# Performance work log

Hardware: AMD Instinct MI355X
Metric: run time of the kernel (lower is better)

The kernel has to match this reference:

```python
import jax, jax.numpy as jnp
import numpy as np

B, NB, NA, F = 4, 262144, 8192, 32

def _mk_mlp(key, d_in):
    ks = jax.random.split(key, 3)
    def lin(k, i, o):
        bound = 1.0 / np.sqrt(i)
        kw, kb = jax.random.split(k)
        w = jax.random.uniform(kw, (i, o), jnp.float32, -bound, bound)
        b = jax.random.uniform(kb, (o,), jnp.float32, -bound, bound)
        return w, b
    w1, b1 = lin(ks[0], d_in, 64)
    w2, b2 = lin(ks[1], 64, 64)
    w3, b3 = lin(ks[2], 64, 32)
    return w1, b1, w2, b2, w3, b3

def setup_inputs() -> dict:
    key = jax.random.key(0)
    ks = jax.random.split(key, 8)
    inp = {
        "bonds": jax.random.normal(ks[0], (B, NB, F), jnp.float32),
        "bond_atom_1": jax.random.randint(ks[1], (B, NB), 0, NA, jnp.int32),
        "bond_atom_2": jax.random.randint(ks[2], (B, NB), 0, NA, jnp.int32),
        "atoms": jax.random.normal(ks[3], (B, NA, F), jnp.float32),
        "state": jax.random.normal(ks[4], (B, 1, F), jnp.float32),
    }
    for name, d_in, k in (("e", 128, ks[5]), ("v", 96, ks[6]), ("u", 96, ks[7])):
        w1, b1, w2, b2, w3, b3 = _mk_mlp(k, d_in)
        inp[f"{name}_w1"], inp[f"{name}_b1"] = w1, b1
        inp[f"{name}_w2"], inp[f"{name}_b2"] = w2, b2
        inp[f"{name}_w3"], inp[f"{name}_b3"] = w3, b3
    return inp

def _mlp(x, w1, b1, w2, b2, w3, b3):
    sp = jax.nn.softplus
    h = sp(x @ w1 + b1)
    h = sp(h @ w2 + b2)
    return sp(h @ w3 + b3)

def reference(bonds, bond_atom_1, bond_atom_2, atoms, state,
              e_w1, e_b1, e_w2, e_b2, e_w3, e_b3,
              v_w1, v_b1, v_w2, v_b2, v_w3, v_b3,
              u_w1, u_b1, u_w2, u_b2, u_w3, u_b3):
    num_atoms = atoms.shape[1]
    num_bonds = bonds.shape[1]
    # gather atom features to bonds: [B, NB, F]
    a1 = jnp.take_along_axis(atoms, bond_atom_1[:, :, None], axis=1)
    a2 = jnp.take_along_axis(atoms, bond_atom_2[:, :, None], axis=1)
    st_b = jnp.broadcast_to(state, (state.shape[0], num_bonds, state.shape[2]))
    e_in = jnp.concatenate([a1, a2, bonds, st_b], axis=2)  # [B, NB, 128]
    bonds_out = _mlp(e_in, e_w1, e_b1, e_w2, e_b2, e_w3, e_b3)  # [B, NB, 32]
    # scatter-add bonds back to atoms with mean (count) normalization
    seg = jax.vmap(lambda s, i: jax.ops.segment_sum(s, i, num_segments=num_atoms))
    bonds_to_atoms = seg(bonds_out, bond_atom_1)  # [B, NA, 32]
    counts = seg(jnp.ones_like(bonds_out[..., :1]), bond_atom_1)  # [B, NA, 1]
    bonds_to_atoms = bonds_to_atoms / counts
    st_a = jnp.broadcast_to(state, (state.shape[0], num_atoms, state.shape[2]))
    v_in = jnp.concatenate([bonds_to_atoms, atoms, st_a], axis=2)  # [B, NA, 96]
    atoms_out = _mlp(v_in, v_w1, v_b1, v_w2, v_b2, v_w3, v_b3)  # [B, NA, 32]
    u_in = jnp.concatenate([
        jnp.mean(bonds_out, axis=1, keepdims=True),
        jnp.mean(atoms_out, axis=1, keepdims=True),
        state], axis=2)  # [B, 1, 96]
    state_out = _mlp(u_in, u_w1, u_b1, u_w2, u_b2, u_w3, u_b3)  # [B, 1, 32]
    return bonds_out, atoms_out, state_out
```

## Files before the change

kernel.cpp:

```cpp
#include <hip/hip_runtime.h>

#define B_   4
#define NB_  262144
#define NA_  8192
#define NB_SHIFT 18

typedef short bf16x8 __attribute__((ext_vector_type(8)));
typedef float f32x4  __attribute__((ext_vector_type(4)));

__device__ __forceinline__ float bflo(unsigned int u){ return __uint_as_float(u << 16); }
__device__ __forceinline__ float bfhi(unsigned int u){ return __uint_as_float(u & 0xffff0000u); }
__device__ __forceinline__ unsigned short f2bf(float f){
  unsigned int u = __float_as_uint(f);
  u += 0x7fffu + ((u >> 16) & 1u);
  return (unsigned short)(u >> 16);
}
__device__ __forceinline__ unsigned int packbf(float a, float b){
  unsigned int r;
  asm("v_cvt_pk_bf16_f32 %0, %1, %2" : "=v"(r) : "v"(a), "v"(b));
  return r;
}
__device__ __forceinline__ float softplus_f(float v){
  return fmaxf(v, 0.0f) + __logf(1.0f + __expf(-fabsf(v)));
}
__device__ __forceinline__ void lds_fence(){
  asm volatile("" ::: "memory");
  __builtin_amdgcn_wave_barrier();
  __builtin_amdgcn_sched_barrier(0);
}

struct WPtrs { const float* p[18]; };

__global__ __launch_bounds__(256) void prep_kernel(WPtrs wp, float* __restrict__ W){
  int i = blockIdx.x * 256 + threadIdx.x;
  if (i >= 39392) return;
  int idx = i;
  const int sizes[18] = {8192,64,4096,64,2048,32,
                         6144,64,4096,64,2048,32,
                         6144,64,4096,64,2048,32};
  #pragma unroll
  for (int s = 0; s < 18; ++s){
    if (idx < sizes[s]){ W[i] = wp.p[s][idx]; return; }
    idx -= sizes[s];
  }
}

__global__ __launch_bounds__(512) void biaseff_kernel(const float* __restrict__ state,
                                                      const float* __restrict__ W,
                                                      float* __restrict__ be,
                                                      float* __restrict__ bv){
  int t = threadIdx.x;
  int b = (t >> 6) & 3, j = t & 63;
  const float* st = state + b*32;
  if (t < 256){
    float a = W[8192 + j];
    #pragma unroll
    for (int k = 0; k < 32; ++k) a = fmaf(st[k], W[(96+k)*64 + j], a);
    be[b*64 + j] = a;
  } else {
    float a = W[14496 + 6144 + j];
    #pragma unroll
    for (int k = 0; k < 32; ++k) a = fmaf(st[k], W[14496 + (64+k)*64 + j], a);
    bv[b*64 + j] = a;
  }
}

__global__ __launch_bounds__(256) void swizzle_kernel(
    const float* __restrict__ ew1, const float* __restrict__ ew2,
    const float* __restrict__ ew3,
    const float* __restrict__ vw1, const float* __restrict__ vw2,
    const float* __restrict__ vw3,
    unsigned short* __restrict__ Wb, unsigned short* __restrict__ Wbv){
  int i = blockIdx.x*256 + threadIdx.x;
  if (i >= 24576) return;
  int j = i & 7, lane = (i >> 3) & 63;
  int quad = lane >> 4, l16 = lane & 15;
  int krow = quad*8 + j;
  float v;
  if (i < 14336){
    if (i < 8192){
      int g = i >> 9;  int mt = g & 3, kt = g >> 2;
      v = ew1[(kt*32 + krow)*64 + mt*16 + l16];
    } else if (i < 12288){
      int g = (i - 8192) >> 9;  int mt = g & 3, kt = g >> 2;
      v = ew2[(kt*32 + krow)*64 + mt*16 + l16];
    } else {
      int g = (i - 12288) >> 9;  int mt = g & 1, kt = g >> 1;
      v = ew3[(kt*32 + krow)*32 + mt*16 + l16];
    }
    Wb[i] = f2bf(v);
  } else {
    int o = i - 14336;
    if (o < 4096){
      int g = o >> 9;  int mt = g & 3, kt = g >> 2;
      v = vw1[(kt*32 + krow)*64 + mt*16 + l16];
    } else if (o < 8192){
      int g = (o - 4096) >> 9;  int mt = g & 3, kt = g >> 2;
      v = vw2[(kt*32 + krow)*64 + mt*16 + l16];
    } else {
      int g = (o - 8192) >> 9;  int mt = g & 1, kt = g >> 1;
      v = vw3[(kt*32 + krow)*32 + mt*16 + l16];
    }
    Wbv[o] = f2bf(v);
  }
}

__global__ __launch_bounds__(1024) void hist_lds_kernel(const int* __restrict__ ba1,
                                                        int* __restrict__ partials){
  __shared__ int lh[NA_];
  const int tid = threadIdx.x;
  const int blk = blockIdx.x;
  const int b = blk >> 4;
  const size_t base = (size_t)b*NB_ + (size_t)(blk & 15)*16384;
  #pragma unroll
  for (int i = tid; i < NA_; i += 1024) lh[i] = 0;
  __syncthreads();
  #pragma unroll
  for (int it = 0; it < 16; ++it)
    atomicAdd(&lh[ba1[base + it*1024 + tid]], 1);
  __syncthreads();
  #pragma unroll
  for (int i = tid; i < NA_; i += 1024) partials[blk*NA_ + i] = lh[i];
}

__global__ __launch_bounds__(256) void reduce_kernel(const int* __restrict__ partials,
                                                     int* __restrict__ counts){
  int t = blockIdx.x*256 + threadIdx.x;
  int b = t >> 13, aa = t & (NA_-1);
  int s = 0;
  #pragma unroll
  for (int lb = 0; lb < 16; ++lb) s += partials[(b*16 + lb)*NA_ + aa];
  counts[t] = s;
}

__global__ __launch_bounds__(1024) void scan_kernel(const int* __restrict__ counts,
                                                    int* __restrict__ offsets){
  __shared__ int s[1024];
  const int tid = threadIdx.x;
  const int base = tid * 32;
  int local[32]; int sum = 0;
  #pragma unroll
  for (int i = 0; i < 32; ++i){ local[i] = counts[base + i]; sum += local[i]; }
  s[tid] = sum;
  __syncthreads();
  for (int off = 1; off < 1024; off <<= 1){
    int v = (tid >= off) ? s[tid - off] : 0;
    __syncthreads();
    s[tid] += v;
    __syncthreads();
  }
  int run = s[tid] - sum;
  #pragma unroll
  for (int i = 0; i < 32; ++i){
    offsets[base + i] = run; run += local[i];
  }
}

__global__ __launch_bounds__(256) void base_kernel(const int* __restrict__ offsets,
                                                   const int* __restrict__ partials,
                                                   int* __restrict__ bases){
  int t = blockIdx.x*256 + threadIdx.x;
  int b = t >> 13, aa = t & (NA_-1);
  int run = offsets[t];
  #pragma unroll
  for (int lb = 0; lb < 16; ++lb){
    int g = (b*16 + lb)*NA_ + aa;
    bases[g] = run; run += partials[g];
  }
}

__global__ __launch_bounds__(1024) void fill_lds_kernel(const int* __restrict__ ba1,
                                                        const int* __restrict__ bases,
                                                        int* __restrict__ list){
  __shared__ int lh[NA_];
  const int tid = threadIdx.x;
  const int blk = blockIdx.x;
  const int b = blk >> 4;
  const size_t base = (size_t)b*NB_ + (size_t)(blk & 15)*16384;
  #pragma unroll
  for (int i = tid; i < NA_; i += 1024) lh[i] = 0;
  __syncthreads();
  #pragma unroll
  for (int it = 0; it < 16; ++it){
    int idx = it*1024 + tid;
    int a = ba1[base + idx];
    int rank = atomicAdd(&lh[a], 1);
    list[bases[blk*NA_ + a] + rank] = (int)((base + idx) & (NB_ - 1));
  }
}

__global__ __launch_bounds__(256, 5) void bonds_kernel(
    const float* __restrict__ bonds,
    const int* __restrict__ ba1,
    const int* __restrict__ ba2,
    const float* __restrict__ atoms,
    const float* __restrict__ W,
    const unsigned short* __restrict__ Wb,
    const float* __restrict__ be,
    float* __restrict__ bonds_out)
{
  __shared__ unsigned short hsall[4][1160];
  const int tid  = threadIdx.x;
  const int wave = tid >> 6, lane = tid & 63;
  const int quad = lane >> 4, l16 = lane & 15;
  const int b = blockIdx.y;
  const int rowbase = blockIdx.x*256 + wave*64;
  unsigned short* hwr = &hsall[wave][0] + l16*72;

  int r[4], g1[4], g2[4];
  #pragma unroll
  for (int nt = 0; nt < 4; ++nt){
    r[nt]  = rowbase + nt*16 + l16;
    g1[nt] = ba1[(size_t)b*NB_ + r[nt]];
    g2[nt] = ba2[(size_t)b*NB_ + r[nt]];
  }

  #pragma unroll
  for (int nt = 0; nt < 4; ++nt){
    f32x4 a1[4] = {};
    #pragma unroll
    for (int kt = 0; kt < 3; ++kt){
      const float* src;
      if      (kt == 0) src = atoms + ((size_t)b*NA_ + g1[nt])*32 + quad*8;
      else if (kt == 1) src = atoms + ((size_t)b*NA_ + g2[nt])*32 + quad*8;
      else              src = bonds + ((size_t)b*NB_ + r[nt])*32 + quad*8;
      float4 v0 = *(const float4*)(src);
      float4 v1 = *(const float4*)(src + 4);
      union { bf16x8 v; unsigned int u[4]; } xf;
      xf.u[0] = packbf(v0.x, v0.y);
      xf.u[1] = packbf(v0.z, v0.w);
      xf.u[2] = packbf(v1.x, v1.y);
      xf.u[3] = packbf(v1.z, v1.w);
      #pragma unroll
      for (int mt = 0; mt < 4; ++mt){
        bf16x8 wf = *(const bf16x8*)(Wb + ((kt*4 + mt)*64 + lane)*8);
        a1[mt] = __builtin_amdgcn_mfma_f32_16x16x32_bf16(wf, xf.v, a1[mt], 0, 0, 0);
      }
    }
    lds_fence();
    #pragma unroll
    for (int mt = 0; mt < 4; ++mt){
      float4 bias = *(const float4*)(be + b*64 + mt*16 + quad*4);
      unsigned int lo = packbf(softplus_f(a1[mt][0] + bias.x), softplus_f(a1[mt][1] + bias.y));
      unsigned int hi = packbf(softplus_f(a1[mt][2] + bias.z), softplus_f(a1[mt][3] + bias.w));
      *reinterpret_cast<uint2*>(hwr + mt*16 + quad*4) = make_uint2(lo, hi);
    }
    lds_fence();

    f32x4 a2[4] = {};
    #pragma unroll
    for (int kt = 0; kt < 2; ++kt){
      bf16x8 hf = *(const bf16x8*)(hwr + kt*32 + quad*8);
      #pragma unroll
      for (int mt = 0; mt < 4; ++mt){
        bf16x8 wf = *(const bf16x8*)(Wb + 8192 + ((kt*4 + mt)*64 + lane)*8);
        a2[mt] = __builtin_amdgcn_mfma_f32_16x16x32_bf16(wf, hf, a2[mt], 0, 0, 0);
      }
    }
    lds_fence();
    #pragma unroll
    for (int mt = 0; mt < 4; ++mt){
      float4 bias = *(const float4*)(W + 12352 + mt*16 + quad*4);
      unsigned int lo = packbf(softplus_f(a2[mt][0] + bias.x), softplus_f(a2[mt][1] + bias.y));
      unsigned int hi = packbf(softplus_f(a2[mt][2] + bias.z), softplus_f(a2[mt][3] + bias.w));
      *reinterpret_cast<uint2*>(hwr + mt*16 + quad*4) = make_uint2(lo, hi);
    }
    lds_fence();

    f32x4 a3[2] = {};
    #pragma unroll
    for (int kt = 0; kt < 2; ++kt){
      bf16x8 hf = *(const bf16x8*)(hwr + kt*32 + quad*8);
      #pragma unroll
      for (int mt = 0; mt < 2; ++mt){
        bf16x8 wf = *(const bf16x8*)(Wb + 12288 + ((kt*2 + mt)*64 + lane)*8);
        a3[mt] = __builtin_amdgcn_mfma_f32_16x16x32_bf16(wf, hf, a3[mt], 0, 0, 0);
      }
    }
    #pragma unroll
    for (int mt = 0; mt < 2; ++mt){
      float4 bias = *(const float4*)(W + 14464 + mt*16 + quad*4);
      float4 o;
      o.x = softplus_f(a3[mt][0] + bias.x);
      o.y = softplus_f(a3[mt][1] + bias.y);
      o.z = softplus_f(a3[mt][2] + bias.z);
      o.w = softplus_f(a3[mt][3] + bias.w);
      *reinterpret_cast<float4*>(bonds_out + ((size_t)b*NB_ + r[nt])*32 + mt*16 + quad*4) = o;
    }
  }
}

__global__ __launch_bounds__(256) void gather_kernel(
    const int* __restrict__ counts,
    const int* __restrict__ offsets,
    const int* __restrict__ list,
    const float* __restrict__ bonds_out,
    unsigned int* __restrict__ btap)
{
  int i = blockIdx.x*256 + threadIdx.x;
  int p = i & 7;
  int row = i >> 3;
  int b = row >> 13;
  int c = counts[row], o = offsets[row];
  const float* basep = bonds_out + (size_t)b*NB_*32 + p*4;
  float4 acc = make_float4(0.f, 0.f, 0.f, 0.f);
  int t = 0;
  for (; t + 2 <= c; t += 2){
    int i0 = list[o+t], i1 = list[o+t+1];
    float4 v0 = *(const float4*)(basep + (size_t)i0*32);
    float4 v1 = *(const float4*)(basep + (size_t)i1*32);
    acc.x += v0.x + v1.x; acc.y += v0.y + v1.y;
    acc.z += v0.z + v1.z; acc.w += v0.w + v1.w;
  }
  if (t < c){
    int i0 = list[o+t];
    float4 v0 = *(const float4*)(basep + (size_t)i0*32);
    acc.x += v0.x; acc.y += v0.y; acc.z += v0.z; acc.w += v0.w;
  }
  float inv = 1.0f / (float)c;
  btap[(size_t)row*16 + p*2    ] = packbf(acc.x*inv, acc.y*inv);
  btap[(size_t)row*16 + p*2 + 1] = packbf(acc.z*inv, acc.w*inv);
}

__global__ __launch_bounds__(256, 5) void atoms_kernel(
    const float* __restrict__ atoms,
    const float* __restrict__ Wv,
    const int* __restrict__ counts,
    const unsigned int* __restrict__ btap,
    const float* __restrict__ bv,
    const unsigned short* __restrict__ Wbv,
    float* __restrict__ atoms_out,
    float* __restrict__ bondsum,
    float* __restrict__ atomsum)
{
  __shared__ unsigned short hsall[4][1160];
  const int tid  = threadIdx.x;
  const int wave = tid >> 6, lane = tid & 63;
  const int quad = lane >> 4, l16 = lane & 15;
  const int b = blockIdx.y;
  const int arowbase = blockIdx.x*256 + wave*64;
  unsigned short* hwr = &hsall[wave][0] + l16*72;

  int arow[4], cnt[4];
  #pragma unroll
  for (int nt = 0; nt < 4; ++nt){
    arow[nt] = b*NA_ + arowbase + nt*16 + l16;
    cnt[nt]  = counts[arow[nt]];
  }

  float p1[8] = {0,0,0,0,0,0,0,0};
  float p2[8] = {0,0,0,0,0,0,0,0};

  #pragma unroll
  for (int nt = 0; nt < 4; ++nt){
    f32x4 a1[4] = {};
    {
      union { uint4 q; bf16x8 v; } bt;
      bt.q = *(const uint4*)(btap + (size_t)arow[nt]*16 + quad*4);
      float cf = (float)cnt[nt];
      p1[0] += bflo(bt.q.x)*cf; p1[1] += bfhi(bt.q.x)*cf;
      p1[2] += bflo(bt.q.y)*cf; p1[3] += bfhi(bt.q.y)*cf;
      p1[4] += bflo(bt.q.z)*cf; p1[5] += bfhi(bt.q.z)*cf;
      p1[6] += bflo(bt.q.w)*cf; p1[7] += bfhi(bt.q.w)*cf;
      #pragma unroll
      for (int mt = 0; mt < 4; ++mt){
        bf16x8 wf = *(const bf16x8*)(Wbv + ((0*4 + mt)*64 + lane)*8);
        a1[mt] = __builtin_amdgcn_mfma_f32_16x16x32_bf16(wf, bt.v, a1[mt], 0, 0, 0);
      }
    }
    {
      const float* src = atoms + (size_t)arow[nt]*32 + quad*8;
      float4 v0 = *(const float4*)(src);
      float4 v1 = *(const float4*)(src + 4);
      union { bf16x8 v; unsigned int u[4]; } xf;
      xf.u[0] = packbf(v0.x, v0.y);
      xf.u[1] = packbf(v0.z, v0.w);
      xf.u[2] = packbf(v1.x, v1.y);
      xf.u[3] = packbf(v1.z, v1.w);
      #pragma unroll
      for (int mt = 0; mt < 4; ++mt){
        bf16x8 wf = *(const bf16x8*)(Wbv + ((1*4 + mt)*64 + lane)*8);
        a1[mt] = __builtin_amdgcn_mfma_f32_16x16x32_bf16(wf, xf.v, a1[mt], 0, 0, 0);
      }
    }
    lds_fence();
    #pragma unroll
    for (int mt = 0; mt < 4; ++mt){
      float4 bias = *(const float4*)(bv + b*64 + mt*16 + quad*4);
      unsigned int lo = packbf(softplus_f(a1[mt][0] + bias.x), softplus_f(a1[mt][1] + bias.y));
      unsigned int hi = packbf(softplus_f(a1[mt][2] + bias.z), softplus_f(a1[mt][3] + bias.w));
      *reinterpret_cast<uint2*>(hwr + mt*16 + quad*4) = make_uint2(lo, hi);
    }
    lds_fence();

    f32x4 a2[4] = {};
    #pragma unroll
    for (int kt = 0; kt < 2; ++kt){
      bf16x8 hf = *(const bf16x8*)(hwr + kt*32 + quad*8);
      #pragma unroll
      for (int mt = 0; mt < 4; ++mt){
        bf16x8 wf = *(const bf16x8*)(Wbv + 4096 + ((kt*4 + mt)*64 + lane)*8);
        a2[mt] = __builtin_amdgcn_mfma_f32_16x16x32_bf16(wf, hf, a2[mt], 0, 0, 0);
      }
    }
    lds_fence();
    #pragma unroll
    for (int mt = 0; mt < 4; ++mt){
      float4 bias = *(const float4*)(Wv + 10304 + mt*16 + quad*4);
      unsigned int lo = packbf(softplus_f(a2[mt][0] + bias.x), softplus_f(a2[mt][1] + bias.y));
      unsigned int hi = packbf(softplus_f(a2[mt][2] + bias.z), softplus_f(a2[mt][3] + bias.w));
      *reinterpret_cast<uint2*>(hwr + mt*16 + quad*4) = make_uint2(lo, hi);
    }
    lds_fence();

    f32x4 a3[2] = {};
    #pragma unroll
    for (int kt = 0; kt < 2; ++kt){
      bf16x8 hf = *(const bf16x8*)(hwr + kt*32 + quad*8);
      #pragma unroll
      for (int mt = 0; mt < 2; ++mt){
        bf16x8 wf = *(const bf16x8*)(Wbv + 8192 + ((kt*2 + mt)*64 + lane)*8);
        a3[mt] = __builtin_amdgcn_mfma_f32_16x16x32_bf16(wf, hf, a3[mt], 0, 0, 0);
      }
    }
    #pragma unroll
    for (int mt = 0; mt < 2; ++mt){
      float4 bias = *(const float4*)(Wv + 12416 + mt*16 + quad*4);
      float4 o;
      o.x = softplus_f(a3[mt][0] + bias.x);
      o.y = softplus_f(a3[mt][1] + bias.y);
      o.z = softplus_f(a3[mt][2] + bias.z);
      o.w = softplus_f(a3[mt][3] + bias.w);
      p2[mt*4+0] += o.x; p2[mt*4+1] += o.y; p2[mt*4+2] += o.z; p2[mt*4+3] += o.w;
      *reinterpret_cast<float4*>(atoms_out + (size_t)arow[nt]*32 + mt*16 + quad*4) = o;
    }
  }

  #pragma unroll
  for (int j = 0; j < 8; ++j){
    float v = p1[j];
    v += __shfl_xor(v, 1); v += __shfl_xor(v, 2);
    v += __shfl_xor(v, 4); v += __shfl_xor(v, 8);
    if (l16 == 0) unsafeAtomicAdd(&bondsum[b*32 + quad*8 + j], v);
    float w = p2[j];
    w += __shfl_xor(w, 1); w += __shfl_xor(w, 2);
    w += __shfl_xor(w, 4); w += __shfl_xor(w, 8);
    if (l16 == 0) unsafeAtomicAdd(&atomsum[b*32 + (j>>2)*16 + quad*4 + (j&3)], w);
  }
}

__global__ __launch_bounds__(256) void state_kernel(
    const float* __restrict__ state,
    const float* __restrict__ W,
    const float* __restrict__ bondsum,
    const float* __restrict__ atomsum,
    float* __restrict__ state_out)
{
  __shared__ float uin[4][96];
  __shared__ float h1s[4][64];
  __shared__ float h2s[4][64];
  const int tid = threadIdx.x;
  const int b = tid >> 6;
  const int j = tid & 63;
  if (j < 32){
    uin[b][j]      = bondsum[b*32 + j] * (1.0f/(float)NB_);
    uin[b][32 + j] = atomsum[b*32 + j] * (1.0f/(float)NA_);
    uin[b][64 + j] = state[(size_t)b*32 + j];
  }
  __syncthreads();
  float a1 = W[6144 + j];
  for (int k = 0; k < 96; ++k) a1 = fmaf(uin[b][k], W[k*64 + j], a1);
  h1s[b][j] = softplus_f(a1);
  __syncthreads();
  float a2 = W[10304 + j];
  for (int k = 0; k < 64; ++k) a2 = fmaf(h1s[b][k], W[6208 + k*64 + j], a2);
  h2s[b][j] = softplus_f(a2);
  __syncthreads();
  if (j < 32){
    float a3 = W[12416 + j];
    for (int k = 0; k < 64; ++k) a3 = fmaf(h2s[b][k], W[10368 + k*32 + j], a3);
    state_out[b*32 + j] = softplus_f(a3);
  }
}

extern "C" void kernel_launch(void* const* d_in, const int* in_sizes, int n_in,
                              void* d_out, int out_size, void* d_ws, size_t ws_size,
                              hipStream_t stream)
{
  (void)in_sizes; (void)n_in; (void)out_size; (void)ws_size;
  const float* bonds = (const float*)d_in[0];
  const int*   ba1   = (const int*)d_in[1];
  const int*   ba2   = (const int*)d_in[2];
  const float* atoms = (const float*)d_in[3];
  const float* state = (const float*)d_in[4];

  int*          counts  = (int*)d_ws;
  int*          offsets = counts + 32768;
  unsigned short* Wbv   = (unsigned short*)((unsigned int*)d_ws + 65536);
  int*          list    = counts + 98304;
  unsigned int* btap    = (unsigned int*)d_ws + 1146880;
  float*        bondsum = (float*)d_ws + 1671168;
  float*        atomsum = (float*)d_ws + 1671296;
  float*        W       = (float*)d_ws + 1671424;
  unsigned short* Wb    = (unsigned short*)((unsigned int*)d_ws + 1710816);
  float*        be      = (float*)d_ws + 1717984;
  float*        bv      = (float*)d_ws + 1718240;

  int* partials = list;
  int* bases    = (int*)btap;

  hipMemsetAsync(bondsum, 0, 256 * sizeof(float), stream);

  WPtrs wp;
  for (int s = 0; s < 18; ++s) wp.p[s] = (const float*)d_in[5 + s];
  prep_kernel<<<154, 256, 0, stream>>>(wp, W);
  biaseff_kernel<<<1, 512, 0, stream>>>(state, W, be, bv);
  swizzle_kernel<<<96, 256, 0, stream>>>((const float*)d_in[5], (const float*)d_in[7],
                                         (const float*)d_in[9],
                                         (const float*)d_in[11], (const float*)d_in[13],
                                         (const float*)d_in[15], Wb, Wbv);

  hist_lds_kernel<<<64, 1024, 0, stream>>>(ba1, partials);
  reduce_kernel<<<128, 256, 0, stream>>>(partials, counts);
  scan_kernel<<<1, 1024, 0, stream>>>(counts, offsets);
  base_kernel<<<128, 256, 0, stream>>>(offsets, partials, bases);
  fill_lds_kernel<<<64, 1024, 0, stream>>>(ba1, bases, list);

  float* out_bonds = (float*)d_out;
  float* out_atoms = out_bonds + (size_t)B_*NB_*32;
  float* out_state = out_atoms + (size_t)B_*NA_*32;

  bonds_kernel<<<dim3(NB_/256, B_), 256, 0, stream>>>(bonds, ba1, ba2, atoms,
                                                      W, Wb, be, out_bonds);
  gather_kernel<<<(B_*NA_*8)/256, 256, 0, stream>>>(counts, offsets, list, out_bonds, btap);
  atoms_kernel<<<dim3(NA_/256, B_), 256, 0, stream>>>(atoms, W + 14496,
                                                      counts, btap, bv, Wbv, out_atoms,
                                                      bondsum, atomsum);
  state_kernel<<<1, 256, 0, stream>>>(state, W + 26944, bondsum, atomsum, out_state);
}
```

Measured before the change: 542.7 us.

## Merge setup kernels, fold count reduction into histogram, restructure MLP loops

Three weight-prep and bias kernels are merged into one launch. The per-block histogram now atomically accumulates global counts, which removes the separate reduce kernel at the cost of an extra memset. The bonds and atoms MLP kernels are restructured to process all four row tiles per layer, so weight fragments are loaded once per layer and stay in registers. This needs a larger LDS buffer and more accumulator registers, and the occupancy hint drops from 5 to 4. The scan loads counts vectorised, and the sched_barrier is removed from the LDS fence.

```diff
diff --git a/kernel.cpp b/kernel.cpp
--- a/kernel.cpp
+++ b/kernel.cpp
@@ -26,87 +26,82 @@
 __device__ __forceinline__ void lds_fence(){
   asm volatile("" ::: "memory");
   __builtin_amdgcn_wave_barrier();
-  __builtin_amdgcn_sched_barrier(0);
 }
 
 struct WPtrs { const float* p[18]; };
 
-__global__ __launch_bounds__(256) void prep_kernel(WPtrs wp, float* __restrict__ W){
-  int i = blockIdx.x * 256 + threadIdx.x;
-  if (i >= 39392) return;
-  int idx = i;
-  const int sizes[18] = {8192,64,4096,64,2048,32,
-                         6144,64,4096,64,2048,32,
-                         6144,64,4096,64,2048,32};
-  #pragma unroll
-  for (int s = 0; s < 18; ++s){
-    if (idx < sizes[s]){ W[i] = wp.p[s][idx]; return; }
-    idx -= sizes[s];
-  }
-}
-
-__global__ __launch_bounds__(512) void biaseff_kernel(const float* __restrict__ state,
-                                                      const float* __restrict__ W,
-                                                      float* __restrict__ be,
-                                                      float* __restrict__ bv){
-  int t = threadIdx.x;
-  int b = (t >> 6) & 3, j = t & 63;
-  const float* st = state + b*32;
-  if (t < 256){
-    float a = W[8192 + j];
-    #pragma unroll
-    for (int k = 0; k < 32; ++k) a = fmaf(st[k], W[(96+k)*64 + j], a);
+__global__ __launch_bounds__(256) void setup_kernel(
+    WPtrs wp, const float* __restrict__ state,
+    float* __restrict__ W,
+    unsigned short* __restrict__ Wb, unsigned short* __restrict__ Wbv,
+    float* __restrict__ be, float* __restrict__ bv)
+{
+  const int blk = blockIdx.x;
+  const int tid = threadIdx.x;
+  if (blk < 154){
+    int i = blk*256 + tid;
+    if (i >= 39392) return;
+    int idx = i;
+    const int sizes[18] = {8192,64,4096,64,2048,32,
+                           6144,64,4096,64,2048,32,
+                           6144,64,4096,64,2048,32};
+    #pragma unroll
+    for (int s = 0; s < 18; ++s){
+      if (idx < sizes[s]){ W[i] = wp.p[s][idx]; return; }
+      idx -= sizes[s];
+    }
+  } else if (blk < 250){
+    int i = (blk - 154)*256 + tid;
+    int j = i & 7, lane = (i >> 3) & 63;
+    int quad = lane >> 4, l16 = lane & 15;
+    int krow = quad*8 + j;
+    float v;
+    if (i < 14336){
+      if (i < 8192){
+        int g = i >> 9;  int mt = g & 3, kt = g >> 2;
+        v = wp.p[0][(kt*32 + krow)*64 + mt*16 + l16];
+      } else if (i < 12288){
+        int g = (i - 8192) >> 9;  int mt = g & 3, kt = g >> 2;
+        v = wp.p[2][(kt*32 + krow)*64 + mt*16 + l16];
+      } else {
+        int g = (i - 12288) >> 9;  int mt = g & 1, kt = g >> 1;
+        v = wp.p[4][(kt*32 + krow)*32 + mt*16 + l16];
+      }
+      Wb[i] = f2bf(v);
+    } else {
+      int o = i - 14336;
+      if (o < 4096){
+        int g = o >> 9;  int mt = g & 3, kt = g >> 2;
+        v = wp.p[6][(kt*32 + krow)*64 + mt*16 + l16];
+      } else if (o < 8192){
+        int g = (o - 4096) >> 9;  int mt = g & 3, kt = g >> 2;
+        v = wp.p[8][(kt*32 + krow)*64 + mt*16 + l16];
+      } else {
+        int g = (o - 8192) >> 9;  int mt = g & 1, kt = g >> 1;
+        v = wp.p[10][(kt*32 + krow)*32 + mt*16 + l16];
+      }
+      Wbv[o] = f2bf(v);
+    }
+  } else if (blk == 250){
+    int b = tid >> 6, j = tid & 63;
+    const float* st = state + b*32;
+    float a = wp.p[1][j];
+    #pragma unroll
+    for (int k = 0; k < 32; ++k) a = fmaf(st[k], wp.p[0][(96+k)*64 + j], a);
     be[b*64 + j] = a;
   } else {
-    float a = W[14496 + 6144 + j];
-    #pragma unroll
-    for (int k = 0; k < 32; ++k) a = fmaf(st[k], W[14496 + (64+k)*64 + j], a);
+    int b = tid >> 6, j = tid & 63;
+    const float* st = state + b*32;
+    float a = wp.p[7][j];
+    #pragma unroll
+    for (int k = 0; k < 32; ++k) a = fmaf(st[k], wp.p[6][(64+k)*64 + j], a);
     bv[b*64 + j] = a;
   }
 }
 
-__global__ __launch_bounds__(256) void swizzle_kernel(
-    const float* __restrict__ ew1, const float* __restrict__ ew2,
-    const float* __restrict__ ew3,
-    const float* __restrict__ vw1, const float* __restrict__ vw2,
-    const float* __restrict__ vw3,
-    unsigned short* __restrict__ Wb, unsigned short* __restrict__ Wbv){
-  int i = blockIdx.x*256 + threadIdx.x;
-  if (i >= 24576) return;
-  int j = i & 7, lane = (i >> 3) & 63;
-  int quad = lane >> 4, l16 = lane & 15;
-  int krow = quad*8 + j;
-  float v;
-  if (i < 14336){
-    if (i < 8192){
-      int g = i >> 9;  int mt = g & 3, kt = g >> 2;
-      v = ew1[(kt*32 + krow)*64 + mt*16 + l16];
-    } else if (i < 12288){
-      int g = (i - 8192) >> 9;  int mt = g & 3, kt = g >> 2;
-      v = ew2[(kt*32 + krow)*64 + mt*16 + l16];
-    } else {
-      int g = (i - 12288) >> 9;  int mt = g & 1, kt = g >> 1;
-      v = ew3[(kt*32 + krow)*32 + mt*16 + l16];
-    }
-    Wb[i] = f2bf(v);
-  } else {
-    int o = i - 14336;
-    if (o < 4096){
-      int g = o >> 9;  int mt = g & 3, kt = g >> 2;
-      v = vw1[(kt*32 + krow)*64 + mt*16 + l16];
-    } else if (o < 8192){
-      int g = (o - 4096) >> 9;  int mt = g & 3, kt = g >> 2;
-      v = vw2[(kt*32 + krow)*64 + mt*16 + l16];
-    } else {
-      int g = (o - 8192) >> 9;  int mt = g & 1, kt = g >> 1;
-      v = vw3[(kt*32 + krow)*32 + mt*16 + l16];
-    }
-    Wbv[o] = f2bf(v);
-  }
-}
-
 __global__ __launch_bounds__(1024) void hist_lds_kernel(const int* __restrict__ ba1,
-                                                        int* __restrict__ partials){
+                                                        int* __restrict__ partials,
+                                                        int* __restrict__ counts){
   __shared__ int lh[NA_];
   const int tid = threadIdx.x;
   const int blk = blockIdx.x;
@@ -120,17 +115,11 @@
     atomicAdd(&lh[ba1[base + it*1024 + tid]], 1);
   __syncthreads();
   #pragma unroll
-  for (int i = tid; i < NA_; i += 1024) partials[blk*NA_ + i] = lh[i];
-}
-
-__global__ __launch_bounds__(256) void reduce_kernel(const int* __restrict__ partials,
-                                                     int* __restrict__ counts){
-  int t = blockIdx.x*256 + threadIdx.x;
-  int b = t >> 13, aa = t & (NA_-1);
-  int s = 0;
-  #pragma unroll
-  for (int lb = 0; lb < 16; ++lb) s += partials[(b*16 + lb)*NA_ + aa];
-  counts[t] = s;
+  for (int i = tid; i < NA_; i += 1024){
+    int v = lh[i];
+    partials[blk*NA_ + i] = v;
+    if (v) atomicAdd(&counts[b*NA_ + i], v);
+  }
 }
 
 __global__ __launch_bounds__(1024) void scan_kernel(const int* __restrict__ counts,
@@ -139,8 +128,14 @@
   const int tid = threadIdx.x;
   const int base = tid * 32;
   int local[32]; int sum = 0;
-  #pragma unroll
-  for (int i = 0; i < 32; ++i){ local[i] = counts[base + i]; sum += local[i]; }
+  const uint4* cp = reinterpret_cast<const uint4*>(counts + base);
+  #pragma unroll
+  for (int q = 0; q < 8; ++q){
+    uint4 v = cp[q];
+    local[q*4+0] = (int)v.x; local[q*4+1] = (int)v.y;
+    local[q*4+2] = (int)v.z; local[q*4+3] = (int)v.w;
+    sum += (int)v.x + (int)v.y + (int)v.z + (int)v.w;
+  }
   s[tid] = sum;
   __syncthreads();
   for (int off = 1; off < 1024; off <<= 1){
@@ -189,7 +184,7 @@
   }
 }
 
-__global__ __launch_bounds__(256, 5) void bonds_kernel(
+__global__ __launch_bounds__(256, 4) void bonds_kernel(
     const float* __restrict__ bonds,
     const int* __restrict__ ba1,
     const int* __restrict__ ba2,
@@ -199,13 +194,13 @@
     const float* __restrict__ be,
     float* __restrict__ bonds_out)
 {
-  __shared__ unsigned short hsall[4][1160];
+  __shared__ unsigned short hred[4][64*72];
   const int tid  = threadIdx.x;
   const int wave = tid >> 6, lane = tid & 63;
   const int quad = lane >> 4, l16 = lane & 15;
   const int b = blockIdx.y;
   const int rowbase = blockIdx.x*256 + wave*64;
-  unsigned short* hwr = &hsall[wave][0] + l16*72;
+  unsigned short* H = &hred[wave][0];
 
   int r[4], g1[4], g2[4];
   #pragma unroll
@@ -215,11 +210,15 @@
     g2[nt] = ba2[(size_t)b*NB_ + r[nt]];
   }
 
-  #pragma unroll
-  for (int nt = 0; nt < 4; ++nt){
-    f32x4 a1[4] = {};
-    #pragma unroll
-    for (int kt = 0; kt < 3; ++kt){
+  f32x4 acc[4][4] = {};
+  #pragma unroll
+  for (int kt = 0; kt < 3; ++kt){
+    bf16x8 wf[4];
+    #pragma unroll
+    for (int mt = 0; mt < 4; ++mt)
+      wf[mt] = *(const bf16x8*)(Wb + ((kt*4 + mt)*64 + lane)*8);
+    #pragma unroll
+    for (int nt = 0; nt < 4; ++nt){
       const float* src;
       if      (kt == 0) src = atoms + ((size_t)b*NA_ + g1[nt])*32 + quad*8;
       else if (kt == 1) src = atoms + ((size_t)b*NA_ + g2[nt])*32 + quad*8;
@@ -232,60 +231,93 @@
       xf.u[2] = packbf(v1.x, v1.y);
       xf.u[3] = packbf(v1.z, v1.w);
       #pragma unroll
-      for (int mt = 0; mt < 4; ++mt){
-        bf16x8 wf = *(const bf16x8*)(Wb + ((kt*4 + mt)*64 + lane)*8);
-        a1[mt] = __builtin_amdgcn_mfma_f32_16x16x32_bf16(wf, xf.v, a1[mt], 0, 0, 0);
+      for (int mt = 0; mt < 4; ++mt)
+        acc[mt][nt] = __builtin_amdgcn_mfma_f32_16x16x32_bf16(wf[mt], xf.v, acc[mt][nt], 0, 0, 0);
+    }
+  }
+  {
+    const float* b1v = be + b*64;
+    #pragma unroll
+    for (int mt = 0; mt < 4; ++mt){
+      float4 bias = *(const float4*)(b1v + mt*16 + quad*4);
+      #pragma unroll
+      for (int nt = 0; nt < 4; ++nt){
+        unsigned int lo = packbf(softplus_f(acc[mt][nt][0] + bias.x),
+                                 softplus_f(acc[mt][nt][1] + bias.y));
+        unsigned int hi = packbf(softplus_f(acc[mt][nt][2] + bias.z),
+                                 softplus_f(acc[mt][nt][3] + bias.w));
+        *reinterpret_cast<uint2*>(H + (nt*16 + l16)*72 + mt*16 + quad*4) = make_uint2(lo, hi);
       }
     }
-    lds_fence();
+  }
+  lds_fence();
+
+  f32x4 acc2[4][4] = {};
+  #pragma unroll
+  for (int kt = 0; kt < 2; ++kt){
+    bf16x8 wf[4];
+    #pragma unroll
+    for (int mt = 0; mt < 4; ++mt)
+      wf[mt] = *(const bf16x8*)(Wb + 8192 + ((kt*4 + mt)*64 + lane)*8);
+    #pragma unroll
+    for (int nt = 0; nt < 4; ++nt){
+      bf16x8 hf = *(const bf16x8*)(H + (nt*16 + l16)*72 + kt*32 + quad*8);
+      #pragma unroll
+      for (int mt = 0; mt < 4; ++mt)
+        acc2[mt][nt] = __builtin_amdgcn_mfma_f32_16x16x32_bf16(wf[mt], hf, acc2[mt][nt], 0, 0, 0);
+    }
+  }
+  lds_fence();
+  {
+    const float* b2v = W + 12352;
     #pragma unroll
     for (int mt = 0; mt < 4; ++mt){
-      float4 bias = *(const float4*)(be + b*64 + mt*16 + quad*4);
-      unsigned int lo = packbf(softplus_f(a1[mt][0] + bias.x), softplus_f(a1[mt][1] + bias.y));
-      unsigned int hi = packbf(softplus_f(a1[mt][2] + bias.z), softplus_f(a1[mt][3] + bias.w));
-      *reinterpret_cast<uint2*>(hwr + mt*16 + quad*4) = make_uint2(lo, hi);
-    }
-    lds_fence();
-
-    f32x4 a2[4] = {};
-    #pragma unroll
-    for (int kt = 0; kt < 2; ++kt){
-      bf16x8 hf = *(const bf16x8*)(hwr + kt*32 + quad*8);
-      #pragma unroll
-      for (int mt = 0; mt < 4; ++mt){
-        bf16x8 wf = *(const bf16x8*)(Wb + 8192 + ((kt*4 + mt)*64 + lane)*8);
-        a2[mt] = __builtin_amdgcn_mfma_f32_16x16x32_bf16(wf, hf, a2[mt], 0, 0, 0);
+      float4 bias = *(const float4*)(b2v + mt*16 + quad*4);
+      #pragma unroll
+      for (int nt = 0; nt < 4; ++nt){
+        unsigned int lo = packbf(softplus_f(acc2[mt][nt][0] + bias.x),
+                                 softplus_f(acc2[mt][nt][1] + bias.y));
+        unsigned int hi = packbf(softplus_f(acc2[mt][nt][2] + bias.z),
+                                 softplus_f(acc2[mt][nt][3] + bias.w));
+        *reinterpret_cast<uint2*>(H + (nt*16 + l16)*72 + mt*16 + quad*4) = make_uint2(lo, hi);
       }
     }
-    lds_fence();
-    #pragma unroll
-    for (int mt = 0; mt < 4; ++mt){
-      float4 bias = *(const float4*)(W + 12352 + mt*16 + quad*4);
-      unsigned int lo = packbf(softplus_f(a2[mt][0] + bias.x), softplus_f(a2[mt][1] + bias.y));
-      unsigned int hi = packbf(softplus_f(a2[mt][2] + bias.z), softplus_f(a2[mt][3] + bias.w));
-      *reinterpret_cast<uint2*>(hwr + mt*16 + quad*4) = make_uint2(lo, hi);
-    }
-    lds_fence();
-
-    f32x4 a3[2] = {};
-    #pragma unroll
-    for (int kt = 0; kt < 2; ++kt){
-      bf16x8 hf = *(const bf16x8*)(hwr + kt*32 + quad*8);
-      #pragma unroll
-      for (int mt = 0; mt < 2; ++mt){
-        bf16x8 wf = *(const bf16x8*)(Wb + 12288 + ((kt*2 + mt)*64 + lane)*8);
-        a3[mt] = __builtin_amdgcn_mfma_f32_16x16x32_bf16(wf, hf, a3[mt], 0, 0, 0);
-      }
-    }
-    #pragma unroll
-    for (int mt = 0; mt < 2; ++mt){
-      float4 bias = *(const float4*)(W + 14464 + mt*16 + quad*4);
-      float4 o;
-      o.x = softplus_f(a3[mt][0] + bias.x);
-      o.y = softplus_f(a3[mt][1] + bias.y);
-      o.z = softplus_f(a3[mt][2] + bias.z);
-      o.w = softplus_f(a3[mt][3] + bias.w);
-      *reinterpret_cast<float4*>(bonds_out + ((size_t)b*NB_ + r[nt])*32 + mt*16 + quad*4) = o;
+  }
+  lds_fence();
+
+  f32x4 acc3[2][4] = {};
+  #pragma unroll
+  for (int kt = 0; kt < 2; ++kt){
+    bf16x8 wf[2];
+    #pragma unroll
+    for (int mt = 0; mt < 2; ++mt)
+      wf[mt] = *(const bf16x8*)(Wb + 12288 + ((kt*2 + mt)*64 + lane)*8);
+    #pragma unroll
+    for (int nt = 0; nt < 4; ++nt){
+      bf16x8 hf = *(const bf16x8*)(H + (nt*16 + l16)*72 + kt*32 + quad*8);
+      #pragma unroll
+      for (int mt = 0; mt < 2; ++mt)
+        acc3[mt][nt] = __builtin_amdgcn_mfma_f32_16x16x32_bf16(wf[mt], hf, acc3[mt][nt], 0, 0, 0);
+    }
+  }
+  {
+    const float* b3v = W + 14464;
+    float4 bias0 = *(const float4*)(b3v + quad*4);
+    float4 bias1 = *(const float4*)(b3v + 16 + quad*4);
+    #pragma unroll
+    for (int nt = 0; nt < 4; ++nt){
+      float4 o0, o1;
+      o0.x = softplus_f(acc3[0][nt][0] + bias0.x);
+      o0.y = softplus_f(acc3[0][nt][1] + bias0.y);
+      o0.z = softplus_f(acc3[0][nt][2] + bias0.z);
+      o0.w = softplus_f(acc3[0][nt][3] + bias0.w);
+      o1.x = softplus_f(acc3[1][nt][0] + bias1.x);
+      o1.y = softplus_f(acc3[1][nt][1] + bias1.y);
+      o1.z = softplus_f(acc3[1][nt][2] + bias1.z);
+      o1.w = softplus_f(acc3[1][nt][3] + bias1.w);
+      float* outp = bonds_out + ((size_t)b*NB_ + r[nt])*32 + quad*4;
+      *reinterpret_cast<float4*>(outp)      = o0;
+      *reinterpret_cast<float4*>(outp + 16) = o1;
     }
   }
 }
@@ -322,7 +354,7 @@
   btap[(size_t)row*16 + p*2 + 1] = packbf(acc.z*inv, acc.w*inv);
 }
 
-__global__ __launch_bounds__(256, 5) void atoms_kernel(
+__global__ __launch_bounds__(256, 4) void atoms_kernel(
     const float* __restrict__ atoms,
     const float* __restrict__ Wv,
     const int* __restrict__ counts,
@@ -333,13 +365,13 @@
     float* __restrict__ bondsum,
     float* __restrict__ atomsum)
 {
-  __shared__ unsigned short hsall[4][1160];
+  __shared__ unsigned short hred[4][64*72];
   const int tid  = threadIdx.x;
   const int wave = tid >> 6, lane = tid & 63;
   const int quad = lane >> 4, l16 = lane & 15;
   const int b = blockIdx.y;
   const int arowbase = blockIdx.x*256 + wave*64;
-  unsigned short* hwr = &hsall[wave][0] + l16*72;
+  unsigned short* H = &hred[wave][0];
 
   int arow[4], cnt[4];
   #pragma unroll
@@ -351,10 +383,14 @@
   float p1[8] = {0,0,0,0,0,0,0,0};
   float p2[8] = {0,0,0,0,0,0,0,0};
 
-  #pragma unroll
-  for (int nt = 0; nt < 4; ++nt){
-    f32x4 a1[4] = {};
-    {
+  f32x4 acc[4][4] = {};
+  {
+    bf16x8 wf[4];
+    #pragma unroll
+    for (int mt = 0; mt < 4; ++mt)
+      wf[mt] = *(const bf16x8*)(Wbv + ((0*4 + mt)*64 + lane)*8);
+    #pragma unroll
+    for (int nt = 0; nt < 4; ++nt){
       union { uint4 q; bf16x8 v; } bt;
       bt.q = *(const uint4*)(btap + (size_t)arow[nt]*16 + quad*4);
       float cf = (float)cnt[nt];
@@ -363,12 +399,17 @@
       p1[4] += bflo(bt.q.z)*cf; p1[5] += bfhi(bt.q.z)*cf;
       p1[6] += bflo(bt.q.w)*cf; p1[7] += bfhi(bt.q.w)*cf;
       #pragma unroll
-      for (int mt = 0; mt < 4; ++mt){
-        bf16x8 wf = *(const bf16x8*)(Wbv + ((0*4 + mt)*64 + lane)*8);
-        a1[mt] = __builtin_amdgcn_mfma_f32_16x16x32_bf16(wf, bt.v, a1[mt], 0, 0, 0);
-      }
-    }
-    {
+      for (int mt = 0; mt < 4; ++mt)
+        acc[mt][nt] = __builtin_amdgcn_mfma_f32_16x16x32_bf16(wf[mt], bt.v, acc[mt][nt], 0, 0, 0);
+    }
+  }
+  {
+    bf16x8 wf[4];
+    #pragma unroll
+    for (int mt = 0; mt < 4; ++mt)
+      wf[mt] = *(const bf16x8*)(Wbv + ((1*4 + mt)*64 + lane)*8);
+    #pragma unroll
+    for (int nt = 0; nt < 4; ++nt){
       const float* src = atoms + (size_t)arow[nt]*32 + quad*8;
       float4 v0 = *(const float4*)(src);
       float4 v1 = *(const float4*)(src + 4);
@@ -378,61 +419,95 @@
       xf.u[2] = packbf(v1.x, v1.y);
       xf.u[3] = packbf(v1.z, v1.w);
       #pragma unroll
-      for (int mt = 0; mt < 4; ++mt){
-        bf16x8 wf = *(const bf16x8*)(Wbv + ((1*4 + mt)*64 + lane)*8);
-        a1[mt] = __builtin_amdgcn_mfma_f32_16x16x32_bf16(wf, xf.v, a1[mt], 0, 0, 0);
+      for (int mt = 0; mt < 4; ++mt)
+        acc[mt][nt] = __builtin_amdgcn_mfma_f32_16x16x32_bf16(wf[mt], xf.v, acc[mt][nt], 0, 0, 0);
+    }
+  }
+  {
+    const float* b1v = bv + b*64;
+    #pragma unroll
+    for (int mt = 0; mt < 4; ++mt){
+      float4 bias = *(const float4*)(b1v + mt*16 + quad*4);
+      #pragma unroll
+      for (int nt = 0; nt < 4; ++nt){
+        unsigned int lo = packbf(softplus_f(acc[mt][nt][0] + bias.x),
+                                 softplus_f(acc[mt][nt][1] + bias.y));
+        unsigned int hi = packbf(softplus_f(acc[mt][nt][2] + bias.z),
+                                 softplus_f(acc[mt][nt][3] + bias.w));
+        *reinterpret_cast<uint2*>(H + (nt*16 + l16)*72 + mt*16 + quad*4) = make_uint2(lo, hi);
       }
     }
-    lds_fence();
+  }
+  lds_fence();
+
+  f32x4 acc2[4][4] = {};
+  #pragma unroll
+  for (int kt = 0; kt < 2; ++kt){
+    bf16x8 wf[4];
+    #pragma unroll
+    for (int mt = 0; mt < 4; ++mt)
+      wf[mt] = *(const bf16x8*)(Wbv + 4096 + ((kt*4 + mt)*64 + lane)*8);
+    #pragma unroll
+    for (int nt = 0; nt < 4; ++nt){
+      bf16x8 hf = *(const bf16x8*)(H + (nt*16 + l16)*72 + kt*32 + quad*8);
+      #pragma unroll
+      for (int mt = 0; mt < 4; ++mt)
+        acc2[mt][nt] = __builtin_amdgcn_mfma_f32_16x16x32_bf16(wf[mt], hf, acc2[mt][nt], 0, 0, 0);
+    }
+  }
+  lds_fence();
+  {
+    const float* b2v = Wv + 10304;
     #pragma unroll
     for (int mt = 0; mt < 4; ++mt){
-      float4 bias = *(const float4*)(bv + b*64 + mt*16 + quad*4);
-      unsigned int lo = packbf(softplus_f(a1[mt][0] + bias.x), softplus_f(a1[mt][1] + bias.y));
-      unsigned int hi = packbf(softplus_f(a1[mt][2] + bias.z), softplus_f(a1[mt][3] + bias.w));
-      *reinterpret_cast<uint2*>(hwr + mt*16 + quad*4) = make_uint2(lo, hi);
-    }
-    lds_fence();
-
-    f32x4 a2[4] = {};
-    #pragma unroll
-    for (int kt = 0; kt < 2; ++kt){
-      bf16x8 hf = *(const bf16x8*)(hwr + kt*32 + quad*8);
-      #pragma unroll
-      for (int mt = 0; mt < 4; ++mt){
-        bf16x8 wf = *(const bf16x8*)(Wbv + 4096 + ((kt*4 + mt)*64 + lane)*8);
-        a2[mt] = __builtin_amdgcn_mfma_f32_16x16x32_bf16(wf, hf, a2[mt], 0, 0, 0);
+      float4 bias = *(const float4*)(b2v + mt*16 + quad*4);
+      #pragma unroll
+      for (int nt = 0; nt < 4; ++nt){
+        unsigned int lo = packbf(softplus_f(acc2[mt][nt][0] + bias.x),
+                                 softplus_f(acc2[mt][nt][1] + bias.y));
+        unsigned int hi = packbf(softplus_f(acc2[mt][nt][2] + bias.z),
+                                 softplus_f(acc2[mt][nt][3] + bias.w));
+        *reinterpret_cast<uint2*>(H + (nt*16 + l16)*72 + mt*16 + quad*4) = make_uint2(lo, hi);
       }
     }
-    lds_fence();
-    #pragma unroll
-    for (int mt = 0; mt < 4; ++mt){
-      float4 bias = *(const float4*)(Wv + 10304 + mt*16 + quad*4);
-      unsigned int lo = packbf(softplus_f(a2[mt][0] + bias.x), softplus_f(a2[mt][1] + bias.y));
-      unsigned int hi = packbf(softplus_f(a2[mt][2] + bias.z), softplus_f(a2[mt][3] + bias.w));
-      *reinterpret_cast<uint2*>(hwr + mt*16 + quad*4) = make_uint2(lo, hi);
-    }
-    lds_fence();
-
-    f32x4 a3[2] = {};
-    #pragma unroll
-    for (int kt = 0; kt < 2; ++kt){
-      bf16x8 hf = *(const bf16x8*)(hwr + kt*32 + quad*8);
-      #pragma unroll
-      for (int mt = 0; mt < 2; ++mt){
-        bf16x8 wf = *(const bf16x8*)(Wbv + 8192 + ((kt*2 + mt)*64 + lane)*8);
-        a3[mt] = __builtin_amdgcn_mfma_f32_16x16x32_bf16(wf, hf, a3[mt], 0, 0, 0);
-      }
-    }
-    #pragma unroll
-    for (int mt = 0; mt < 2; ++mt){
-      float4 bias = *(const float4*)(Wv + 12416 + mt*16 + quad*4);
-      float4 o;
-      o.x = softplus_f(a3[mt][0] + bias.x);
-      o.y = softplus_f(a3[mt][1] + bias.y);
-      o.z = softplus_f(a3[mt][2] + bias.z);
-      o.w = softplus_f(a3[mt][3] + bias.w);
-      p2[mt*4+0] += o.x; p2[mt*4+1] += o.y; p2[mt*4+2] += o.z; p2[mt*4+3] += o.w;
-      *reinterpret_cast<float4*>(atoms_out + (size_t)arow[nt]*32 + mt*16 + quad*4) = o;
+  }
+  lds_fence();
+
+  f32x4 acc3[2][4] = {};
+  #pragma unroll
+  for (int kt = 0; kt < 2; ++kt){
+    bf16x8 wf[2];
+    #pragma unroll
+    for (int mt = 0; mt < 2; ++mt)
+      wf[mt] = *(const bf16x8*)(Wbv + 8192 + ((kt*2 + mt)*64 + lane)*8);
+    #pragma unroll
+    for (int nt = 0; nt < 4; ++nt){
+      bf16x8 hf = *(const bf16x8*)(H + (nt*16 + l16)*72 + kt*32 + quad*8);
+      #pragma unroll
+      for (int mt = 0; mt < 2; ++mt)
+        acc3[mt][nt] = __builtin_amdgcn_mfma_f32_16x16x32_bf16(wf[mt], hf, acc3[mt][nt], 0, 0, 0);
+    }
+  }
+  {
+    const float* b3v = Wv + 12416;
+    float4 bias0 = *(const float4*)(b3v + quad*4);
+    float4 bias1 = *(const float4*)(b3v + 16 + quad*4);
+    #pragma unroll
+    for (int nt = 0; nt < 4; ++nt){
+      float4 o0, o1;
+      o0.x = softplus_f(acc3[0][nt][0] + bias0.x);
+      o0.y = softplus_f(acc3[0][nt][1] + bias0.y);
+      o0.z = softplus_f(acc3[0][nt][2] + bias0.z);
+      o0.w = softplus_f(acc3[0][nt][3] + bias0.w);
+      o1.x = softplus_f(acc3[1][nt][0] + bias1.x);
+      o1.y = softplus_f(acc3[1][nt][1] + bias1.y);
+      o1.z = softplus_f(acc3[1][nt][2] + bias1.z);
+      o1.w = softplus_f(acc3[1][nt][3] + bias1.w);
+      p2[0] += o0.x; p2[1] += o0.y; p2[2] += o0.z; p2[3] += o0.w;
+      p2[4] += o1.x; p2[5] += o1.y; p2[6] += o1.z; p2[7] += o1.w;
+      float* outp = atoms_out + (size_t)arow[nt]*32 + quad*4;
+      *reinterpret_cast<float4*>(outp)      = o0;
+      *reinterpret_cast<float4*>(outp + 16) = o1;
     }
   }
 
@@ -509,19 +584,14 @@
   int* partials = list;
   int* bases    = (int*)btap;
 
+  hipMemsetAsync(counts, 0, 32768 * sizeof(int), stream);
   hipMemsetAsync(bondsum, 0, 256 * sizeof(float), stream);
 
   WPtrs wp;
   for (int s = 0; s < 18; ++s) wp.p[s] = (const float*)d_in[5 + s];
-  prep_kernel<<<154, 256, 0, stream>>>(wp, W);
-  biaseff_kernel<<<1, 512, 0, stream>>>(state, W, be, bv);
-  swizzle_kernel<<<96, 256, 0, stream>>>((const float*)d_in[5], (const float*)d_in[7],
-                                         (const float*)d_in[9],
-                                         (const float*)d_in[11], (const float*)d_in[13],
-                                         (const float*)d_in[15], Wb, Wbv);
-
-  hist_lds_kernel<<<64, 1024, 0, stream>>>(ba1, partials);
-  reduce_kernel<<<128, 256, 0, stream>>>(partials, counts);
+  setup_kernel<<<252, 256, 0, stream>>>(wp, state, W, Wb, Wbv, be, bv);
+
+  hist_lds_kernel<<<64, 1024, 0, stream>>>(ba1, partials, counts);
   scan_kernel<<<1, 1024, 0, stream>>>(counts, offsets);
   base_kernel<<<128, 256, 0, stream>>>(offsets, partials, bases);
   fill_lds_kernel<<<64, 1024, 0, stream>>>(ba1, bases, list);
```

Result: faster. 491.4 us (-9.5%).
